# Kernel tuning notes

Hardware: AMD Instinct MI355X
Metric: run time of the kernel (lower is better)

Reference implementation:

```python
import jax, jax.numpy as jnp
import numpy as np

N_AGENTS = 8

def _nearest(x, codebook):
    # x: [N, D], codebook: [K, D] -> indices [N]
    # squared L2 distance via expansion; argmin over codebook axis
    d2 = (jnp.sum(x * x, axis=1, keepdims=True)
          - 2.0 * x @ codebook.T
          + jnp.sum(codebook * codebook, axis=1)[None, :])  # [N, K]
    return jnp.argmin(d2, axis=1)

def setup_inputs() -> dict:
    key = jax.random.key(0)
    ks = jax.random.split(key, 16)
    s = 0.02
    H, D_in, R, K, S = 512, 256, 64, 256, 512
    inp = {
        "inputs": jax.random.normal(ks[0], (131072, D_in), jnp.float32),
        "W0": jax.random.normal(ks[1], (D_in, H), jnp.float32) * s,
        "b0": jnp.zeros((H,), jnp.float32),
        "W1": jax.random.normal(ks[2], (H, H), jnp.float32) * s,
        "b1": jnp.zeros((H,), jnp.float32),
        "W2": jax.random.normal(ks[3], (H, R), jnp.float32) * s,
        "b2": jnp.zeros((R,), jnp.float32),
        "codebook": jax.random.normal(ks[4], (K, R), jnp.float32),
        "W3": jax.random.normal(ks[5], (R, H), jnp.float32) * s,
        "b3": jnp.zeros((H,), jnp.float32),
        "W4": jax.random.normal(ks[6], (N_AGENTS * H, H), jnp.float32) * s,
        "b4": jnp.zeros((H,), jnp.float32),
        "W5": jax.random.normal(ks[7], (H, S), jnp.float32) * s,
        "b5": jnp.zeros((S,), jnp.float32),
    }
    return inp

def reference(inputs, W0, b0, W1, b1, W2, b2, codebook, W3, b3, W4, b4, W5, b5):
    # encode: fc2(relu(fc1(relu(fc0(x)))))
    h = jax.nn.relu(inputs @ W0 + b0)
    h = jax.nn.relu(h @ W1 + b1)
    z_e = h @ W2 + b2  # [N, role_dim]

    # emb(z_e, weight_sg=True): straight-through to z_e, codebook detached
    idx1 = _nearest(z_e, codebook)
    z_q_raw = jnp.take(codebook, idx1, axis=0)
    z_q = z_e + jax.lax.stop_gradient(z_q_raw - z_e)

    # emb(z_e.detach()): grad flows to codebook only (gather -> scatter-add vjp)
    z_e_sg = jax.lax.stop_gradient(z_e)
    idx2 = _nearest(z_e_sg, codebook)
    role_emb = jnp.take(codebook, idx2, axis=0)

    # decode
    rec = jax.nn.relu(z_q @ W3 + b3).reshape(-1, N_AGENTS * W3.shape[1])
    rec = jax.nn.relu(rec @ W4 + b4)
    recon = rec @ W5 + b5  # [N/n_agents, state_dim]
    return recon, z_e, role_emb
```

## Files before the change

kernel.cpp:

```cpp
#include <hip/hip_runtime.h>
#include <hip/hip_bf16.h>
#include <cstddef>

__device__ __forceinline__ unsigned short f2bf(float f) {
    union { float f; unsigned int u; } v; v.f = f;
    unsigned int r = (v.u + 0x7fffu + ((v.u >> 16) & 1u)) >> 16;
    return (unsigned short)r;
}

typedef __bf16    bf16x8 __attribute__((ext_vector_type(8)));
typedef float     f32x4  __attribute__((ext_vector_type(4)));
typedef _Float16  f16x8  __attribute__((ext_vector_type(8)));

#define SPLIT_SCALE 2.44140625e-4f

typedef const __attribute__((address_space(1))) void cglb_t;
typedef __attribute__((address_space(3))) void lds_t;

__device__ __forceinline__ void fsplit(float v, _Float16& hi, _Float16& lo) {
    hi = (_Float16)v;
    lo = (_Float16)((v - (float)hi) * 4096.0f);
}

__device__ __forceinline__ int swz4(int r) { return (r & 3) ^ ((r >> 2) & 3); }

template<int K>
__global__ __launch_bounds__(256, 3)
void gemm_split7(const _Float16* __restrict__ Ahi, const _Float16* __restrict__ Alo,
                 const _Float16* __restrict__ Bhi, const _Float16* __restrict__ Blo,
                 const float* __restrict__ bias,
                 _Float16* __restrict__ Chi, _Float16* __restrict__ Clo,
                 int M, int N)
{
    constexpr int BK = 32;
    constexpr int NS = K / BK;

    __shared__ alignas(16) _Float16 SA[2][2][128 * 32];
    __shared__ alignas(16) _Float16 SB[2][2][64 * 32];

    const int tid  = threadIdx.x;
    const int lane = tid & 63;
    const int w    = tid >> 6;

    int bx = blockIdx.x, by = blockIdx.y;
    {
        const int gx = gridDim.x, nwg = gx * gridDim.y;
        if ((nwg & 7) == 0) {
            int d = bx + by * gx;
            int L = (d & 7) * (nwg >> 3) + (d >> 3);
            bx = L % gx; by = L / gx;
        }
    }
    const int bm = by * 128;
    const int bn = bx * 64;

    f32x4 acc0[2][4], acc1[2][4];
#pragma unroll
    for (int m = 0; m < 2; ++m)
#pragma unroll
        for (int n = 0; n < 4; ++n) {
            acc0[m][n] = (f32x4){0.f, 0.f, 0.f, 0.f};
            acc1[m][n] = (f32x4){0.f, 0.f, 0.f, 0.f};
        }

    auto stage = [&](int buf, int k0) {
#pragma unroll
        for (int pl = 0; pl < 2; ++pl) {
            const _Float16* src = pl ? Alo : Ahi;
#pragma unroll
            for (int j = 0; j < 2; ++j) {
                const int p16 = (w * 2 + j) * 64 + lane;
                const int r   = p16 >> 2;
                const int c   = (p16 & 3) ^ swz4(r);
                const _Float16* g = src + (size_t)(bm + r) * K + k0 + c * 8;
                __builtin_amdgcn_global_load_lds((cglb_t*)g,
                    (lds_t*)&SA[buf][pl][p16 * 8], 16, 0, 0);
            }
            const _Float16* srcB = pl ? Blo : Bhi;
            const int p16b = w * 64 + lane;
            const int rb   = p16b >> 2;
            const int cb   = (p16b & 3) ^ swz4(rb);
            const _Float16* gB = srcB + (size_t)(bn + rb) * K + k0 + cb * 8;
            __builtin_amdgcn_global_load_lds((cglb_t*)gB,
                (lds_t*)&SB[buf][pl][p16b * 8], 16, 0, 0);
        }
    };

    stage(0, 0);
    __syncthreads();

    const int g   = lane >> 4;
    const int r15 = lane & 15;

#pragma unroll
    for (int s = 0; s < NS; ++s) {
        const int p = s & 1;
        if (s + 1 < NS) stage(p ^ 1, (s + 1) * BK);

        f16x8 ah[2], al[2];
#pragma unroll
        for (int m = 0; m < 2; ++m) {
            const int R = w * 32 + m * 16 + r15;
            const int a16 = R * 4 + (g ^ swz4(R));
            ah[m] = *reinterpret_cast<const f16x8*>(&SA[p][0][a16 * 8]);
            al[m] = *reinterpret_cast<const f16x8*>(&SA[p][1][a16 * 8]);
        }
#pragma unroll
        for (int n = 0; n < 4; ++n) {
            const int rB = n * 16 + r15;
            const int b16 = rB * 4 + (g ^ swz4(rB));
            const f16x8 bh = *reinterpret_cast<const f16x8*>(&SB[p][0][b16 * 8]);
            const f16x8 bl = *reinterpret_cast<const f16x8*>(&SB[p][1][b16 * 8]);
#pragma unroll
            for (int m = 0; m < 2; ++m)
                acc0[m][n] = __builtin_amdgcn_mfma_f32_16x16x32_f16(
                    ah[m], bh, acc0[m][n], 0, 0, 0);
#pragma unroll
            for (int m = 0; m < 2; ++m)
                acc1[m][n] = __builtin_amdgcn_mfma_f32_16x16x32_f16(
                    ah[m], bl, acc1[m][n], 0, 0, 0);
#pragma unroll
            for (int m = 0; m < 2; ++m)
                acc1[m][n] = __builtin_amdgcn_mfma_f32_16x16x32_f16(
                    al[m], bh, acc1[m][n], 0, 0, 0);
        }
        __syncthreads();
    }

#pragma unroll
    for (int m = 0; m < 2; ++m)
#pragma unroll
        for (int n = 0; n < 4; ++n) {
            const int col = bn + n * 16 + r15;
            const float bv = bias[col];
#pragma unroll
            for (int q = 0; q < 4; ++q) {
                const int row = bm + w * 32 + m * 16 + (lane >> 4) * 4 + q;
                float v = acc0[m][n][q] + SPLIT_SCALE * acc1[m][n][q] + bv;
                v = fmaxf(v, 0.f);
                _Float16 hi, lo; fsplit(v, hi, lo);
                Chi[(size_t)row * N + col] = hi;
                Clo[(size_t)row * N + col] = lo;
            }
        }
}

template<bool RELU, bool OUT_BF16>
__global__ __launch_bounds__(256, 3)
void gemm_bt7(const unsigned short* __restrict__ A,
              const unsigned short* __restrict__ Bt,
              const float* __restrict__ bias,
              void* __restrict__ Cv, int M, int N, int K)
{
    constexpr int BK = 32;

    __shared__ alignas(16) unsigned short SA[2][128 * 32];
    __shared__ alignas(16) unsigned short SB[2][128 * 32];

    const int tid  = threadIdx.x;
    const int lane = tid & 63;
    const int w    = tid >> 6;
    const int wr   = (w >> 1) * 64;
    const int wc   = (w & 1) * 64;

    int bx = blockIdx.x, by = blockIdx.y;
    {
        const int gx = gridDim.x, nwg = gx * gridDim.y;
        if ((nwg & 7) == 0) {
            int d = bx + by * gx;
            int L = (d & 7) * (nwg >> 3) + (d >> 3);
            bx = L % gx; by = L / gx;
        }
    }
    const int bm = by * 128;
    const int bn = bx * 128;

    f32x4 acc[4][4];
#pragma unroll
    for (int m = 0; m < 4; ++m)
#pragma unroll
        for (int n = 0; n < 4; ++n) acc[m][n] = (f32x4){0.f, 0.f, 0.f, 0.f};

    auto stage = [&](int buf, int k0) {
#pragma unroll
        for (int j = 0; j < 2; ++j) {
            const int p16 = (w * 2 + j) * 64 + lane;
            const int r   = p16 >> 2;
            const int c   = (p16 & 3) ^ swz4(r);
            const unsigned short* gA = A + (size_t)(bm + r) * K + k0 + c * 8;
            __builtin_amdgcn_global_load_lds((cglb_t*)gA,
                (lds_t*)&SA[buf][p16 * 8], 16, 0, 0);
            const unsigned short* gB = Bt + (size_t)(bn + r) * K + k0 + c * 8;
            __builtin_amdgcn_global_load_lds((cglb_t*)gB,
                (lds_t*)&SB[buf][p16 * 8], 16, 0, 0);
        }
    };

    stage(0, 0);
    __syncthreads();

    const int g   = lane >> 4;
    const int r15 = lane & 15;
    const int NS  = K / BK;

    for (int s = 0; s < NS; ++s) {
        const int p = s & 1;
        if (s + 1 < NS) stage(p ^ 1, (s + 1) * BK);

        bf16x8 af[4], bf[4];
#pragma unroll
        for (int m = 0; m < 4; ++m) {
            const int R = wr + m * 16 + r15;
            const int a16 = R * 4 + (g ^ swz4(R));
            af[m] = *reinterpret_cast<const bf16x8*>(&SA[p][a16 * 8]);
        }
#pragma unroll
        for (int n = 0; n < 4; ++n) {
            const int RB = wc + n * 16 + r15;
            const int b16 = RB * 4 + (g ^ swz4(RB));
            bf[n] = *reinterpret_cast<const bf16x8*>(&SB[p][b16 * 8]);
        }
#pragma unroll
        for (int m = 0; m < 4; ++m)
#pragma unroll
            for (int n = 0; n < 4; ++n)
                acc[m][n] = __builtin_amdgcn_mfma_f32_16x16x32_bf16(
                    af[m], bf[n], acc[m][n], 0, 0, 0);
        __syncthreads();
    }

#pragma unroll
    for (int m = 0; m < 4; ++m)
#pragma unroll
        for (int n = 0; n < 4; ++n) {
            const int col = bn + wc + n * 16 + r15;
            const float bv = bias[col];
#pragma unroll
            for (int q = 0; q < 4; ++q) {
                const int row = bm + wr + m * 16 + (lane >> 4) * 4 + q;
                float v = acc[m][n][q] + bv;
                if (RELU) v = fmaxf(v, 0.f);
                if (OUT_BF16)
                    reinterpret_cast<unsigned short*>(Cv)[(size_t)row * N + col] = f2bf(v);
                else
                    reinterpret_cast<float*>(Cv)[(size_t)row * N + col] = v;
            }
        }
}

template<int K, bool AF32>
__global__ __launch_bounds__(256, AF32 ? 3 : 4)
void gemm_split5(const void* __restrict__ Asrc,
                 const _Float16* __restrict__ Bhi, const _Float16* __restrict__ Blo,
                 const float* __restrict__ bias,
                 _Float16* __restrict__ Chi, _Float16* __restrict__ Clo,
                 int M, int N)
{
    constexpr int BK  = 32;
    constexpr int LDP = 40;
    constexpr int NS  = K / BK;

    __shared__ alignas(16) _Float16 Bh[2][64][LDP];
    __shared__ alignas(16) _Float16 Bl[2][64][LDP];

    const int tid  = threadIdx.x;
    const int lane = tid & 63;
    const int w    = tid >> 6;

    int bx = blockIdx.x, by = blockIdx.y;
    {
        const int gx = gridDim.x, nwg = gx * gridDim.y;
        if ((nwg & 7) == 0) {
            int d = bx + by * gx;
            int L = (d & 7) * (nwg >> 3) + (d >> 3);
            bx = L % gx; by = L / gx;
        }
    }
    const int bm = by * 128;
    const int bn = bx * 64;

    f32x4 acc0[2][4], acc1[2][4];
#pragma unroll
    for (int m = 0; m < 2; ++m)
#pragma unroll
        for (int n = 0; n < 4; ++n) {
            acc0[m][n] = (f32x4){0.f, 0.f, 0.f, 0.f};
            acc1[m][n] = (f32x4){0.f, 0.f, 0.f, 0.f};
        }

    const int arow = bm + w * 32 + (lane & 15);
    const int kgrp = (lane >> 4) * 8;
    const int brow = tid >> 2;
    const int bcol = (tid & 3) * 8;

    const _Float16* Ahi_ = (const _Float16*)Asrc;
    const float*    Af_  = (const float*)Asrc;

    f16x8 ah[2], al[2], ahn[2], aln[2];
    float4 rbh, rbl;

    auto loadB = [&](int k0) {
        const size_t gb = (size_t)(bn + brow) * K + k0 + bcol;
        rbh = *reinterpret_cast<const float4*>(Bhi + gb);
        rbl = *reinterpret_cast<const float4*>(Blo + gb);
    };
    auto storeB = [&](int p) {
        *reinterpret_cast<float4*>(&Bh[p][brow][bcol]) = rbh;
        *reinterpret_cast<float4*>(&Bl[p][brow][bcol]) = rbl;
    };
    auto loadA = [&](int k0, f16x8* h, f16x8* l) {
#pragma unroll
        for (int m = 0; m < 2; ++m) {
            const size_t ga = (size_t)(arow + m * 16) * K + k0 + kgrp;
            if constexpr (AF32) {
                float4 v0 = *reinterpret_cast<const float4*>(Af_ + ga);
                float4 v1 = *reinterpret_cast<const float4*>(Af_ + ga + 4);
                float vv[8] = {v0.x, v0.y, v0.z, v0.w, v1.x, v1.y, v1.z, v1.w};
                f16x8 hh, ll;
#pragma unroll
                for (int j = 0; j < 8; ++j) {
                    _Float16 hi, lo; fsplit(vv[j], hi, lo);
                    hh[j] = hi; ll[j] = lo;
                }
                h[m] = hh; l[m] = ll;
            } else {
                h[m] = *reinterpret_cast<const f16x8*>(Ahi_ + ga);
                l[m] = *reinterpret_cast<const f16x8*>(Ahi_ + (size_t)M * K + ga);
            }
        }
    };

    loadB(0);
    loadA(0, ah, al);
    storeB(0);
    __syncthreads();

#pragma unroll
    for (int s = 0; s < NS; ++s) {
        const int p = s & 1;
        if (s + 1 < NS) {
            loadB((s + 1) * BK);
            loadA((s + 1) * BK, ahn, aln);
        }
#pragma unroll
        for (int n = 0; n < 4; ++n) {
            const f16x8 bh = *reinterpret_cast<const f16x8*>(
                &Bh[p][n * 16 + (lane & 15)][kgrp]);
            const f16x8 bl = *reinterpret_cast<const f16x8*>(
                &Bl[p][n * 16 + (lane & 15)][kgrp]);
#pragma unroll
            for (int m = 0; m < 2; ++m)
                acc0[m][n] = __builtin_amdgcn_mfma_f32_16x16x32_f16(
                    ah[m], bh, acc0[m][n], 0, 0, 0);
#pragma unroll
            for (int m = 0; m < 2; ++m)
                acc1[m][n] = __builtin_amdgcn_mfma_f32_16x16x32_f16(
                    ah[m], bl, acc1[m][n], 0, 0, 0);
#pragma unroll
            for (int m = 0; m < 2; ++m)
                acc1[m][n] = __builtin_amdgcn_mfma_f32_16x16x32_f16(
                    al[m], bh, acc1[m][n], 0, 0, 0);
        }
        if (s + 1 < NS) {
            storeB(p ^ 1);
#pragma unroll
            for (int m = 0; m < 2; ++m) { ah[m] = ahn[m]; al[m] = aln[m]; }
        }
        __syncthreads();
    }

#pragma unroll
    for (int m = 0; m < 2; ++m)
#pragma unroll
        for (int n = 0; n < 4; ++n) {
            const int col = bn + n * 16 + (lane & 15);
            const float bv = bias[col];
#pragma unroll
            for (int q = 0; q < 4; ++q) {
                const int row = bm + w * 32 + m * 16 + (lane >> 4) * 4 + q;
                float v = acc0[m][n][q] + SPLIT_SCALE * acc1[m][n][q] + bv;
                v = fmaxf(v, 0.f);
                _Float16 hi, lo; fsplit(v, hi, lo);
                Chi[(size_t)row * N + col] = hi;
                Clo[(size_t)row * N + col] = lo;
            }
        }
}

__global__ __launch_bounds__(256)
void gemm_ze_mfma(const _Float16* __restrict__ Ahi, const _Float16* __restrict__ Alo,
                  const _Float16* __restrict__ Bhi, const _Float16* __restrict__ Blo,
                  const float* __restrict__ bias, float* __restrict__ C, int M)
{
    constexpr int K = 512, N = 64;
    const int tid  = threadIdx.x;
    const int lane = tid & 63;
    const int w    = tid >> 6;
    const int wr   = (w >> 1) * 64;
    const int wc   = (w & 1) * 32;
    const int bm   = blockIdx.x * 128;

    f32x4 acc0[4][2], acc1[4][2];
#pragma unroll
    for (int m = 0; m < 4; ++m)
#pragma unroll
        for (int n = 0; n < 2; ++n) {
            acc0[m][n] = (f32x4){0.f, 0.f, 0.f, 0.f};
            acc1[m][n] = (f32x4){0.f, 0.f, 0.f, 0.f};
        }

    const int arow = bm + wr + (lane & 15);
    const int kgrp = (lane >> 4) * 8;

#pragma unroll
    for (int ks = 0; ks < K / 32; ++ks) {
        const int k0 = ks * 32 + kgrp;
        f16x8 ah[4], al[4];
#pragma unroll
        for (int m = 0; m < 4; ++m) {
            const size_t ga = (size_t)(arow + m * 16) * K + k0;
            ah[m] = *reinterpret_cast<const f16x8*>(Ahi + ga);
            al[m] = *reinterpret_cast<const f16x8*>(Alo + ga);
        }
#pragma unroll
        for (int n = 0; n < 2; ++n) {
            const size_t gb = (size_t)(wc + n * 16 + (lane & 15)) * K + k0;
            const f16x8 bh = *reinterpret_cast<const f16x8*>(Bhi + gb);
            const f16x8 bl = *reinterpret_cast<const f16x8*>(Blo + gb);
#pragma unroll
            for (int m = 0; m < 4; ++m)
                acc0[m][n] = __builtin_amdgcn_mfma_f32_16x16x32_f16(
                    ah[m], bh, acc0[m][n], 0, 0, 0);
#pragma unroll
            for (int m = 0; m < 4; ++m)
                acc1[m][n] = __builtin_amdgcn_mfma_f32_16x16x32_f16(
                    ah[m], bl, acc1[m][n], 0, 0, 0);
#pragma unroll
            for (int m = 0; m < 4; ++m)
                acc1[m][n] = __builtin_amdgcn_mfma_f32_16x16x32_f16(
                    al[m], bh, acc1[m][n], 0, 0, 0);
        }
    }

#pragma unroll
    for (int m = 0; m < 4; ++m)
#pragma unroll
        for (int n = 0; n < 2; ++n) {
            const int col = wc + n * 16 + (lane & 15);
            const float bv = bias[col];
#pragma unroll
            for (int q = 0; q < 4; ++q) {
                const int row = bm + wr + m * 16 + (lane >> 4) * 4 + q;
                C[(size_t)row * N + col] = acc0[m][n][q] + SPLIT_SCALE * acc1[m][n][q] + bv;
            }
        }
}

#define VQ_EPS 1e-3f
__global__ __launch_bounds__(512)
void vq_mfma(const float* __restrict__ Z, const float* __restrict__ CB,
             const _Float16* __restrict__ Chi, const _Float16* __restrict__ Clo,
             float* __restrict__ OUT, unsigned short* __restrict__ ZQB)
{
    __shared__ float  ccf[256];
    __shared__ double ccd[256];
    __shared__ float  xxf[128];
    __shared__ double xxd[128];
    __shared__ float  redv[4][128];
    __shared__ int    redi[4][128];
    __shared__ float  bv1s[128];
    __shared__ int    bis[128];
    __shared__ int    cand[128][16];
    __shared__ int    ncand[128];
    __shared__ int    fullflag[128];
    __shared__ int    flaglist[128];
    __shared__ int    nflag;

    const int tid  = threadIdx.x;
    const int lane = tid & 63;
    const int w    = tid >> 6;
    const int wr   = (w >> 2) * 64;
    const int wc   = (w & 3) * 64;
    const int bm   = blockIdx.x * 128;

    if (tid == 0) nflag = 0;
    if (tid < 256) {
        const float4* c4 = reinterpret_cast<const float4*>(CB + (size_t)tid * 64);
        double cc = 0.0;
#pragma unroll
        for (int v = 0; v < 16; ++v) {
            float4 f = c4[v];
            cc = fma((double)f.x, (double)f.x, cc);
            cc = fma((double)f.y, (double)f.y, cc);
            cc = fma((double)f.z, (double)f.z, cc);
            cc = fma((double)f.w, (double)f.w, cc);
        }
        ccd[tid] = cc; ccf[tid] = (float)cc;
    }
    if (tid < 128) {
        const float4* z4 = reinterpret_cast<const float4*>(Z + (size_t)(bm + tid) * 64);
        double xx = 0.0;
#pragma unroll
        for (int v = 0; v < 16; ++v) {
            float4 f = z4[v];
            xx = fma((double)f.x, (double)f.x, xx);
            xx = fma((double)f.y, (double)f.y, xx);
            xx = fma((double)f.z, (double)f.z, xx);
            xx = fma((double)f.w, (double)f.w, xx);
        }
        xxd[tid] = xx; xxf[tid] = (float)xx;
        ncand[tid] = 0; fullflag[tid] = 0;
    }
    __syncthreads();

    f32x4 acc0[4][4], acc1[4][4];
#pragma unroll
    for (int m = 0; m < 4; ++m)
#pragma unroll
        for (int n = 0; n < 4; ++n) {
            acc0[m][n] = (f32x4){0.f, 0.f, 0.f, 0.f};
            acc1[m][n] = (f32x4){0.f, 0.f, 0.f, 0.f};
        }

    const int arow = bm + wr + (lane & 15);
    const int kgrp = (lane >> 4) * 8;

#pragma unroll
    for (int ks = 0; ks < 2; ++ks) {
        const int k0 = ks * 32 + kgrp;
        f16x8 ah[4], al[4];
#pragma unroll
        for (int m = 0; m < 4; ++m) {
            const float* src = Z + (size_t)(arow + m * 16) * 64 + k0;
            float4 v0 = *reinterpret_cast<const float4*>(src);
            float4 v1 = *reinterpret_cast<const float4*>(src + 4);
            float vv[8] = {v0.x, v0.y, v0.z, v0.w, v1.x, v1.y, v1.z, v1.w};
            f16x8 hh, ll;
#pragma unroll
            for (int j = 0; j < 8; ++j) {
                _Float16 hi, lo; fsplit(vv[j], hi, lo);
                hh[j] = hi; ll[j] = lo;
            }
            ah[m] = hh; al[m] = ll;
        }
#pragma unroll
        for (int n = 0; n < 4; ++n) {
            const size_t gb = (size_t)(wc + n * 16 + (lane & 15)) * 64 + k0;
            const f16x8 bh = *reinterpret_cast<const f16x8*>(Chi + gb);
            const f16x8 bl = *reinterpret_cast<const f16x8*>(Clo + gb);
#pragma unroll
            for (int m = 0; m < 4; ++m)
                acc0[m][n] = __builtin_amdgcn_mfma_f32_16x16x32_f16(
                    ah[m], bh, acc0[m][n], 0, 0, 0);
#pragma unroll
            for (int m = 0; m < 4; ++m)
                acc1[m][n] = __builtin_amdgcn_mfma_f32_16x16x32_f16(
                    ah[m], bl, acc1[m][n], 0, 0, 0);
#pragma unroll
            for (int m = 0; m < 4; ++m)
                acc1[m][n] = __builtin_amdgcn_mfma_f32_16x16x32_f16(
                    al[m], bh, acc1[m][n], 0, 0, 0);
        }
    }

#pragma unroll
    for (int m = 0; m < 4; ++m)
#pragma unroll
        for (int n = 0; n < 4; ++n) {
            const int col = wc + n * 16 + (lane & 15);
            const float cf = ccf[col];
#pragma unroll
            for (int q = 0; q < 4; ++q) {
                const int rl = wr + m * 16 + (lane >> 4) * 4 + q;
                float dot = acc0[m][n][q] + SPLIT_SCALE * acc1[m][n][q];
                acc0[m][n][q] = (xxf[rl] - 2.0f * dot) + cf;
            }
        }

    float bvr[4][4]; int bir[4][4];
#pragma unroll
    for (int m = 0; m < 4; ++m)
#pragma unroll
        for (int q = 0; q < 4; ++q) {
            float bv = 3.4e38f; int bi = 0;
#pragma unroll
            for (int n = 0; n < 4; ++n) {
                const int col = wc + n * 16 + (lane & 15);
                const float v = acc0[m][n][q];
                if (v < bv || (v == bv && col < bi)) { bv = v; bi = col; }
            }
            bvr[m][q] = bv; bir[m][q] = bi;
        }
#pragma unroll
    for (int mask = 1; mask < 16; mask <<= 1) {
#pragma unroll
        for (int m = 0; m < 4; ++m)
#pragma unroll
            for (int q = 0; q < 4; ++q) {
                float ov = __shfl_xor(bvr[m][q], mask);
                int   oi = __shfl_xor(bir[m][q], mask);
                if (ov < bvr[m][q] || (ov == bvr[m][q] && oi < bir[m][q])) {
                    bvr[m][q] = ov; bir[m][q] = oi;
                }
            }
    }
    if ((lane & 15) == 0) {
#pragma unroll
        for (int m = 0; m < 4; ++m)
#pragma unroll
            for (int q = 0; q < 4; ++q) {
                const int rl = wr + m * 16 + (lane >> 4) * 4 + q;
                redv[w & 3][rl] = bvr[m][q];
                redi[w & 3][rl] = bir[m][q];
            }
    }
    __syncthreads();

    if (tid < 128) {
        float bv = 3.4e38f; int bi = 0;
#pragma unroll
        for (int nw = 0; nw < 4; ++nw) {
            float v = redv[nw][tid];
            if (v < bv) { bv = v; bi = redi[nw][tid]; }
        }
        bv1s[tid] = bv; bis[tid] = bi;
    }
    __syncthreads();

#pragma unroll
    for (int m = 0; m < 4; ++m)
#pragma unroll
        for (int q = 0; q < 4; ++q) {
            const int rl = wr + m * 16 + (lane >> 4) * 4 + q;
            const float thr = bv1s[rl] + VQ_EPS;
#pragma unroll
            for (int n = 0; n < 4; ++n) {
                const int col = wc + n * 16 + (lane & 15);
                if (acc0[m][n][q] <= thr) {
                    int s = atomicAdd(&ncand[rl], 1);
                    if (s < 16) cand[rl][s] = col;
                    else        fullflag[rl] = 1;
                }
            }
        }
    __syncthreads();

    if (tid < 128) {
        const int nc_ = ncand[tid] < 16 ? ncand[tid] : 16;
        if (nc_ > 1 && !fullflag[tid]) {
            const float4* z4p = reinterpret_cast<const float4*>(Z + (size_t)(bm + tid) * 64);
            const double xx = xxd[tid];
            double best = 1.0e300; int bi = 256;
            for (int s = 0; s < nc_; ++s) {
                const int e = cand[tid][s];
                const float4* c4p = reinterpret_cast<const float4*>(CB + (size_t)e * 64);
                double dot = 0.0;
#pragma unroll
                for (int v = 0; v < 16; ++v) {
                    float4 zf = z4p[v], cf4 = c4p[v];
                    dot = fma((double)zf.x, (double)cf4.x, dot);
                    dot = fma((double)zf.y, (double)cf4.y, dot);
                    dot = fma((double)zf.z, (double)cf4.z, dot);
                    dot = fma((double)zf.w, (double)cf4.w, dot);
                }
                double d2x = (xx - 2.0 * dot) + ccd[e];
                if (d2x < best || (d2x == best && e < bi)) { best = d2x; bi = e; }
            }
            bis[tid] = bi;
        }
        if (fullflag[tid]) {
            int s = atomicAdd(&nflag, 1);
            flaglist[s] = tid;
        }
    }
    __syncthreads();

    for (int fi = w; fi < nflag; fi += 8) {
        const int rl = flaglist[fi];
        const float* zr = Z + (size_t)(bm + rl) * 64;
        const double xx = xxd[rl];
        double best = 1.0e300; int bi = 256;
#pragma unroll
        for (int j = 0; j < 4; ++j) {
            const int e = lane + j * 64;
            const float* c = CB + (size_t)e * 64;
            double dot = 0.0;
#pragma unroll
            for (int d = 0; d < 64; ++d)
                dot = fma((double)zr[d], (double)c[d], dot);
            double d2x = (xx - 2.0 * dot) + ccd[e];
            if (d2x < best || (d2x == best && e < bi)) { best = d2x; bi = e; }
        }
#pragma unroll
        for (int mask = 1; mask < 64; mask <<= 1) {
            double ov = __shfl_xor(best, mask);
            int    oi = __shfl_xor(bi, mask);
            if (ov < best || (ov == best && oi < bi)) { best = ov; bi = oi; }
        }
        if (lane == 0) bis[rl] = bi;
    }
    __syncthreads();

    {
        const int row  = tid >> 2;
        const int part = tid & 3;
        const int bi   = bis[row];
        const float4* src = reinterpret_cast<const float4*>(CB + (size_t)bi * 64) + part * 4;
        float* dst = OUT + (size_t)(bm + row) * 64 + part * 16;
        unsigned short* dq = ZQB + (size_t)(bm + row) * 64 + part * 16;
#pragma unroll
        for (int v = 0; v < 4; ++v) {
            float4 f = src[v];
            *reinterpret_cast<float4*>(dst + v * 4) = f;
            ushort4 qb = { f2bf(f.x), f2bf(f.y), f2bf(f.z), f2bf(f.w) };
            *reinterpret_cast<ushort4*>(dq + v * 4) = qb;
        }
    }
}

__global__ __launch_bounds__(256)
void transpose_bf16(const float* __restrict__ W, unsigned short* __restrict__ Wt,
                    int K, int N)
{
    int idx = blockIdx.x * 256 + threadIdx.x;
    if (idx >= K * N) return;
    int n = idx / K, k = idx % K;
    Wt[idx] = f2bf(W[(size_t)k * N + n]);
}

__global__ __launch_bounds__(256)
void transpose_split_f16(const float* __restrict__ W,
                         _Float16* __restrict__ Whi, _Float16* __restrict__ Wlo,
                         int K, int N)
{
    int idx = blockIdx.x * 256 + threadIdx.x;
    if (idx >= K * N) return;
    int n = idx / K, k = idx % K;
    _Float16 hi, lo; fsplit(W[(size_t)k * N + n], hi, lo);
    Whi[idx] = hi; Wlo[idx] = lo;
}

__global__ __launch_bounds__(256)
void split_flat_f16(const float* __restrict__ src,
                    _Float16* __restrict__ hi, _Float16* __restrict__ lo, int n)
{
    int i = blockIdx.x * 256 + threadIdx.x;
    if (i >= n) return;
    _Float16 h, l; fsplit(src[i], h, l);
    hi[i] = h; lo[i] = l;
}

extern "C" void kernel_launch(void* const* d_in, const int* in_sizes, int n_in,
                              void* d_out, int out_size, void* d_ws, size_t ws_size,
                              hipStream_t stream)
{
    const float* X  = (const float*)d_in[0];
    const float* W0 = (const float*)d_in[1];
    const float* b0 = (const float*)d_in[2];
    const float* W1 = (const float*)d_in[3];
    const float* b1 = (const float*)d_in[4];
    const float* W2 = (const float*)d_in[5];
    const float* b2 = (const float*)d_in[6];
    const float* CB = (const float*)d_in[7];
    const float* W3 = (const float*)d_in[8];
    const float* b3 = (const float*)d_in[9];
    const float* W4 = (const float*)d_in[10];
    const float* b4 = (const float*)d_in[11];
    const float* W5 = (const float*)d_in[12];
    const float* b5 = (const float*)d_in[13];

    const int D_in = 256, H = 512, R = 64, S = 512, NA = 8;
    const int Mtot = in_sizes[0] / D_in;

    float* recon = (float*)d_out;
    float* ze    = recon + (size_t)(Mtot / NA) * S;
    float* remb  = ze + (size_t)Mtot * R;

    char* p = (char*)d_ws;
    _Float16* W0hi = (_Float16*)p;  p += (size_t)H * D_in * 2;
    _Float16* W0lo = (_Float16*)p;  p += (size_t)H * D_in * 2;
    _Float16* W1hi = (_Float16*)p;  p += (size_t)H * H * 2;
    _Float16* W1lo = (_Float16*)p;  p += (size_t)H * H * 2;
    _Float16* W2thi = (_Float16*)p; p += (size_t)R * H * 2;
    _Float16* W2tlo = (_Float16*)p; p += (size_t)R * H * 2;
    _Float16* CBhi = (_Float16*)p;  p += (size_t)256 * R * 2;
    _Float16* CBlo = (_Float16*)p;  p += (size_t)256 * R * 2;
    unsigned short* W3t = (unsigned short*)p;  p += (size_t)H * R * 2;
    unsigned short* W4t = (unsigned short*)p;  p += (size_t)H * (NA * H) * 2;
    unsigned short* W5t = (unsigned short*)p;  p += (size_t)S * H * 2;
    size_t fixed = (size_t)(p - (char*)d_ws);
    fixed = (fixed + 255) & ~(size_t)255;

    int nc = 1;
    while (nc < 128) {
        size_t rpcT = (size_t)Mtot / nc;
        if (fixed + rpcT * 4224 + 1024 <= ws_size) break;
        nc *= 2;
    }
    const int rpc = Mtot / nc;
    char* q = (char*)d_ws + fixed;
    _Float16* h0hi = (_Float16*)q;                 q += (size_t)rpc * H * 2;
    _Float16* h0lo = (_Float16*)q;                 q += (size_t)rpc * H * 2;
    _Float16* h1hi = (_Float16*)q;                 q += (size_t)rpc * H * 2;
    _Float16* h1lo = (_Float16*)q;                 q += (size_t)rpc * H * 2;
    unsigned short* zqb = (unsigned short*)q;      q += (size_t)rpc * R * 2;
    unsigned short* rec1b = (unsigned short*)h0hi;
    unsigned short* rec2b = (unsigned short*)h1hi;

    transpose_split_f16<<<(H * D_in + 255) / 256, 256, 0, stream>>>(W0, W0hi, W0lo, D_in, H);
    transpose_split_f16<<<(H * H + 255) / 256, 256, 0, stream>>>(W1, W1hi, W1lo, H, H);
    transpose_split_f16<<<(H * R + 255) / 256, 256, 0, stream>>>(W2, W2thi, W2tlo, H, R);
    split_flat_f16<<<(256 * R + 255) / 256, 256, 0, stream>>>(CB, CBhi, CBlo, 256 * R);
    transpose_bf16<<<(H * R + 255) / 256, 256, 0, stream>>>(W3, W3t, R, H);
    transpose_bf16<<<(H * NA * H + 255) / 256, 256, 0, stream>>>(W4, W4t, NA * H, H);
    transpose_bf16<<<(S * H + 255) / 256, 256, 0, stream>>>(W5, W5t, H, S);

    for (int r0 = 0; r0 < Mtot; r0 += rpc) {
        const int M6 = rpc / NA;
        gemm_split5<256, true><<<dim3(H / 64, rpc / 128), 256, 0, stream>>>(
            X + (size_t)r0 * D_in, W0hi, W0lo, b0, h0hi, h0lo, rpc, H);
        gemm_split7<512><<<dim3(H / 64, rpc / 128), 256, 0, stream>>>(
            h0hi, h0lo, W1hi, W1lo, b1, h1hi, h1lo, rpc, H);
        gemm_ze_mfma<<<rpc / 128, 256, 0, stream>>>(
            h1hi, h1lo, W2thi, W2tlo, b2, ze + (size_t)r0 * R, rpc);
        vq_mfma<<<rpc / 128, 512, 0, stream>>>(
            ze + (size_t)r0 * R, CB, CBhi, CBlo,
            remb + (size_t)r0 * R, zqb);
        gemm_bt7<true, true><<<dim3(H / 128, rpc / 128), 256, 0, stream>>>(
            zqb, W3t, b3, rec1b, rpc, H, R);
        gemm_bt7<true, true><<<dim3(H / 128, M6 / 128), 256, 0, stream>>>(
            rec1b, W4t, b4, rec2b, M6, H, NA * H);
        gemm_bt7<false, false><<<dim3(S / 128, M6 / 128), 256, 0, stream>>>(
            rec2b, W5t, b5, recon + (size_t)(r0 / NA) * S, M6, S, H);
    }
}
```

Baseline: 945.8 us.

## Stage fp32 A tiles through swizzled LDS for first layer; split decode into larger chunks

After: 855.0 us. -9.6%, faster.

```diff
diff --git a/kernel.cpp b/kernel.cpp
--- a/kernel.cpp
+++ b/kernel.cpp
@@ -145,6 +145,151 @@
         }
 }
 
+__global__ __launch_bounds__(256, 3)
+void gemm_split7f(const float* __restrict__ Af,
+                  const _Float16* __restrict__ Bhi, const _Float16* __restrict__ Blo,
+                  const float* __restrict__ bias,
+                  _Float16* __restrict__ Chi, _Float16* __restrict__ Clo,
+                  int M, int N)
+{
+    constexpr int K  = 256;
+    constexpr int BK = 32;
+    constexpr int NS = K / BK;
+
+    __shared__ alignas(16) _Float16 SA[2][2][128 * 32];
+    __shared__ alignas(16) _Float16 SB[2][2][64 * 32];
+
+    const int tid  = threadIdx.x;
+    const int lane = tid & 63;
+    const int w    = tid >> 6;
+
+    int bx = blockIdx.x, by = blockIdx.y;
+    {
+        const int gx = gridDim.x, nwg = gx * gridDim.y;
+        if ((nwg & 7) == 0) {
+            int d = bx + by * gx;
+            int L = (d & 7) * (nwg >> 3) + (d >> 3);
+            bx = L % gx; by = L / gx;
+        }
+    }
+    const int bm = by * 128;
+    const int bn = bx * 64;
+
+    f32x4 acc0[2][4], acc1[2][4];
+#pragma unroll
+    for (int m = 0; m < 2; ++m)
+#pragma unroll
+        for (int n = 0; n < 4; ++n) {
+            acc0[m][n] = (f32x4){0.f, 0.f, 0.f, 0.f};
+            acc1[m][n] = (f32x4){0.f, 0.f, 0.f, 0.f};
+        }
+
+    float4 ra[2][2];
+    auto loadA = [&](int k0) {
+#pragma unroll
+        for (int j = 0; j < 2; ++j) {
+            const int p16 = tid * 2 + j;
+            const int r   = p16 >> 2;
+            const int c   = (p16 & 3) ^ swz4(r);
+            const float* g = Af + (size_t)(bm + r) * K + k0 + c * 8;
+            ra[j][0] = *reinterpret_cast<const float4*>(g);
+            ra[j][1] = *reinterpret_cast<const float4*>(g + 4);
+        }
+    };
+    auto writeA = [&](int buf) {
+#pragma unroll
+        for (int j = 0; j < 2; ++j) {
+            const int p16 = tid * 2 + j;
+            float vv[8] = {ra[j][0].x, ra[j][0].y, ra[j][0].z, ra[j][0].w,
+                           ra[j][1].x, ra[j][1].y, ra[j][1].z, ra[j][1].w};
+            f16x8 hh, ll;
+#pragma unroll
+            for (int e = 0; e < 8; ++e) {
+                _Float16 hi, lo; fsplit(vv[e], hi, lo);
+                hh[e] = hi; ll[e] = lo;
+            }
+            *reinterpret_cast<f16x8*>(&SA[buf][0][p16 * 8]) = hh;
+            *reinterpret_cast<f16x8*>(&SA[buf][1][p16 * 8]) = ll;
+        }
+    };
+    auto stageB = [&](int buf, int k0) {
+#pragma unroll
+        for (int pl = 0; pl < 2; ++pl) {
+            const _Float16* srcB = pl ? Blo : Bhi;
+            const int p16b = w * 64 + lane;
+            const int rb   = p16b >> 2;
+            const int cb   = (p16b & 3) ^ swz4(rb);
+            const _Float16* gB = srcB + (size_t)(bn + rb) * K + k0 + cb * 8;
+            __builtin_amdgcn_global_load_lds((cglb_t*)gB,
+                (lds_t*)&SB[buf][pl][p16b * 8], 16, 0, 0);
+        }
+    };
+
+    loadA(0);
+    stageB(0, 0);
+    writeA(0);
+    __syncthreads();
+
+    const int g   = lane >> 4;
+    const int r15 = lane & 15;
+
+#pragma unroll
+    for (int s = 0; s < NS; ++s) {
+        const int p = s & 1;
+        if (s + 1 < NS) {
+            stageB(p ^ 1, (s + 1) * BK);
+            loadA((s + 1) * BK);
+        }
+
+        f16x8 ah[2], al[2];
+#pragma unroll
+        for (int m = 0; m < 2; ++m) {
+            const int R = w * 32 + m * 16 + r15;
+            const int a16 = R * 4 + (g ^ swz4(R));
+            ah[m] = *reinterpret_cast<const f16x8*>(&SA[p][0][a16 * 8]);
+            al[m] = *reinterpret_cast<const f16x8*>(&SA[p][1][a16 * 8]);
+        }
+#pragma unroll
+        for (int n = 0; n < 4; ++n) {
+            const int rB = n * 16 + r15;
+            const int b16 = rB * 4 + (g ^ swz4(rB));
+            const f16x8 bh = *reinterpret_cast<const f16x8*>(&SB[p][0][b16 * 8]);
+            const f16x8 bl = *reinterpret_cast<const f16x8*>(&SB[p][1][b16 * 8]);
+#pragma unroll
+            for (int m = 0; m < 2; ++m)
+                acc0[m][n] = __builtin_amdgcn_mfma_f32_16x16x32_f16(
+                    ah[m], bh, acc0[m][n], 0, 0, 0);
+#pragma unroll
+            for (int m = 0; m < 2; ++m)
+                acc1[m][n] = __builtin_amdgcn_mfma_f32_16x16x32_f16(
+                    ah[m], bl, acc1[m][n], 0, 0, 0);
+#pragma unroll
+            for (int m = 0; m < 2; ++m)
+                acc1[m][n] = __builtin_amdgcn_mfma_f32_16x16x32_f16(
+                    al[m], bh, acc1[m][n], 0, 0, 0);
+        }
+        if (s + 1 < NS) writeA(p ^ 1);
+        __syncthreads();
+    }
+
+#pragma unroll
+    for (int m = 0; m < 2; ++m)
+#pragma unroll
+        for (int n = 0; n < 4; ++n) {
+            const int col = bn + n * 16 + r15;
+            const float bv = bias[col];
+#pragma unroll
+            for (int q = 0; q < 4; ++q) {
+                const int row = bm + w * 32 + m * 16 + (lane >> 4) * 4 + q;
+                float v = acc0[m][n][q] + SPLIT_SCALE * acc1[m][n][q] + bv;
+                v = fmaxf(v, 0.f);
+                _Float16 hi, lo; fsplit(v, hi, lo);
+                Chi[(size_t)row * N + col] = hi;
+                Clo[(size_t)row * N + col] = lo;
+            }
+        }
+}
+
 template<bool RELU, bool OUT_BF16>
 __global__ __launch_bounds__(256, 3)
 void gemm_bt7(const unsigned short* __restrict__ A,
@@ -244,145 +389,6 @@
                     reinterpret_cast<unsigned short*>(Cv)[(size_t)row * N + col] = f2bf(v);
                 else
                     reinterpret_cast<float*>(Cv)[(size_t)row * N + col] = v;
-            }
-        }
-}
-
-template<int K, bool AF32>
-__global__ __launch_bounds__(256, AF32 ? 3 : 4)
-void gemm_split5(const void* __restrict__ Asrc,
-                 const _Float16* __restrict__ Bhi, const _Float16* __restrict__ Blo,
-                 const float* __restrict__ bias,
-                 _Float16* __restrict__ Chi, _Float16* __restrict__ Clo,
-                 int M, int N)
-{
-    constexpr int BK  = 32;
-    constexpr int LDP = 40;
-    constexpr int NS  = K / BK;
-
-    __shared__ alignas(16) _Float16 Bh[2][64][LDP];
-    __shared__ alignas(16) _Float16 Bl[2][64][LDP];
-
-    const int tid  = threadIdx.x;
-    const int lane = tid & 63;
-    const int w    = tid >> 6;
-
-    int bx = blockIdx.x, by = blockIdx.y;
-    {
-        const int gx = gridDim.x, nwg = gx * gridDim.y;
-        if ((nwg & 7) == 0) {
-            int d = bx + by * gx;
-            int L = (d & 7) * (nwg >> 3) + (d >> 3);
-            bx = L % gx; by = L / gx;
-        }
-    }
-    const int bm = by * 128;
-    const int bn = bx * 64;
-
-    f32x4 acc0[2][4], acc1[2][4];
-#pragma unroll
-    for (int m = 0; m < 2; ++m)
-#pragma unroll
-        for (int n = 0; n < 4; ++n) {
-            acc0[m][n] = (f32x4){0.f, 0.f, 0.f, 0.f};
-            acc1[m][n] = (f32x4){0.f, 0.f, 0.f, 0.f};
-        }
-
-    const int arow = bm + w * 32 + (lane & 15);
-    const int kgrp = (lane >> 4) * 8;
-    const int brow = tid >> 2;
-    const int bcol = (tid & 3) * 8;
-
-    const _Float16* Ahi_ = (const _Float16*)Asrc;
-    const float*    Af_  = (const float*)Asrc;
-
-    f16x8 ah[2], al[2], ahn[2], aln[2];
-    float4 rbh, rbl;
-
-    auto loadB = [&](int k0) {
-        const size_t gb = (size_t)(bn + brow) * K + k0 + bcol;
-        rbh = *reinterpret_cast<const float4*>(Bhi + gb);
-        rbl = *reinterpret_cast<const float4*>(Blo + gb);
-    };
-    auto storeB = [&](int p) {
-        *reinterpret_cast<float4*>(&Bh[p][brow][bcol]) = rbh;
-        *reinterpret_cast<float4*>(&Bl[p][brow][bcol]) = rbl;
-    };
-    auto loadA = [&](int k0, f16x8* h, f16x8* l) {
-#pragma unroll
-        for (int m = 0; m < 2; ++m) {
-            const size_t ga = (size_t)(arow + m * 16) * K + k0 + kgrp;
-            if constexpr (AF32) {
-                float4 v0 = *reinterpret_cast<const float4*>(Af_ + ga);
-                float4 v1 = *reinterpret_cast<const float4*>(Af_ + ga + 4);
-                float vv[8] = {v0.x, v0.y, v0.z, v0.w, v1.x, v1.y, v1.z, v1.w};
-                f16x8 hh, ll;
-#pragma unroll
-                for (int j = 0; j < 8; ++j) {
-                    _Float16 hi, lo; fsplit(vv[j], hi, lo);
-                    hh[j] = hi; ll[j] = lo;
-                }
-                h[m] = hh; l[m] = ll;
-            } else {
-                h[m] = *reinterpret_cast<const f16x8*>(Ahi_ + ga);
-                l[m] = *reinterpret_cast<const f16x8*>(Ahi_ + (size_t)M * K + ga);
-            }
-        }
-    };
-
-    loadB(0);
-    loadA(0, ah, al);
-    storeB(0);
-    __syncthreads();
-
-#pragma unroll
-    for (int s = 0; s < NS; ++s) {
-        const int p = s & 1;
-        if (s + 1 < NS) {
-            loadB((s + 1) * BK);
-            loadA((s + 1) * BK, ahn, aln);
-        }
-#pragma unroll
-        for (int n = 0; n < 4; ++n) {
-            const f16x8 bh = *reinterpret_cast<const f16x8*>(
-                &Bh[p][n * 16 + (lane & 15)][kgrp]);
-            const f16x8 bl = *reinterpret_cast<const f16x8*>(
-                &Bl[p][n * 16 + (lane & 15)][kgrp]);
-#pragma unroll
-            for (int m = 0; m < 2; ++m)
-                acc0[m][n] = __builtin_amdgcn_mfma_f32_16x16x32_f16(
-                    ah[m], bh, acc0[m][n], 0, 0, 0);
-#pragma unroll
-            for (int m = 0; m < 2; ++m)
-                acc1[m][n] = __builtin_amdgcn_mfma_f32_16x16x32_f16(
-                    ah[m], bl, acc1[m][n], 0, 0, 0);
-#pragma unroll
-            for (int m = 0; m < 2; ++m)
-                acc1[m][n] = __builtin_amdgcn_mfma_f32_16x16x32_f16(
-                    al[m], bh, acc1[m][n], 0, 0, 0);
-        }
-        if (s + 1 < NS) {
-            storeB(p ^ 1);
-#pragma unroll
-            for (int m = 0; m < 2; ++m) { ah[m] = ahn[m]; al[m] = aln[m]; }
-        }
-        __syncthreads();
-    }
-
-#pragma unroll
-    for (int m = 0; m < 2; ++m)
-#pragma unroll
-        for (int n = 0; n < 4; ++n) {
-            const int col = bn + n * 16 + (lane & 15);
-            const float bv = bias[col];
-#pragma unroll
-            for (int q = 0; q < 4; ++q) {
-                const int row = bm + w * 32 + m * 16 + (lane >> 4) * 4 + q;
-                float v = acc0[m][n][q] + SPLIT_SCALE * acc1[m][n][q] + bv;
-                v = fmaxf(v, 0.f);
-                _Float16 hi, lo; fsplit(v, hi, lo);
-                Chi[(size_t)row * N + col] = hi;
-                Clo[(size_t)row * N + col] = lo;
             }
         }
 }
@@ -788,24 +794,29 @@
     unsigned short* W3t = (unsigned short*)p;  p += (size_t)H * R * 2;
     unsigned short* W4t = (unsigned short*)p;  p += (size_t)H * (NA * H) * 2;
     unsigned short* W5t = (unsigned short*)p;  p += (size_t)S * H * 2;
+    unsigned short* zqb = (unsigned short*)p;  p += (size_t)Mtot * R * 2;
     size_t fixed = (size_t)(p - (char*)d_ws);
     fixed = (fixed + 255) & ~(size_t)255;
 
     int nc = 1;
     while (nc < 128) {
         size_t rpcT = (size_t)Mtot / nc;
-        if (fixed + rpcT * 4224 + 1024 <= ws_size) break;
+        if (fixed + rpcT * 4096 + 1024 <= ws_size) break;
         nc *= 2;
     }
     const int rpc = Mtot / nc;
-    char* q = (char*)d_ws + fixed;
-    _Float16* h0hi = (_Float16*)q;                 q += (size_t)rpc * H * 2;
-    _Float16* h0lo = (_Float16*)q;                 q += (size_t)rpc * H * 2;
-    _Float16* h1hi = (_Float16*)q;                 q += (size_t)rpc * H * 2;
-    _Float16* h1lo = (_Float16*)q;                 q += (size_t)rpc * H * 2;
-    unsigned short* zqb = (unsigned short*)q;      q += (size_t)rpc * R * 2;
-    unsigned short* rec1b = (unsigned short*)h0hi;
-    unsigned short* rec2b = (unsigned short*)h1hi;
+    char* regionA = (char*)d_ws + fixed;
+    char* regionB = regionA + (size_t)rpc * 2048;
+
+    _Float16* h1hi = (_Float16*)regionA;
+    _Float16* h1lo = h1hi + (size_t)rpc * H;
+    _Float16* h0hi = (_Float16*)regionB;
+    _Float16* h0lo = h0hi + (size_t)rpc * H;
+
+    int dc = (nc >= 2) ? nc / 2 : 1;
+    const int Mdec = Mtot / dc;
+    unsigned short* rec1b = (unsigned short*)regionB;
+    unsigned short* rec2b = (unsigned short*)regionA;
 
     transpose_split_f16<<<(H * D_in + 255) / 256, 256, 0, stream>>>(W0, W0hi, W0lo, D_in, H);
     transpose_split_f16<<<(H * H + 255) / 256, 256, 0, stream>>>(W1, W1hi, W1lo, H, H);
@@ -816,8 +827,7 @@
     transpose_bf16<<<(S * H + 255) / 256, 256, 0, stream>>>(W5, W5t, H, S);
 
     for (int r0 = 0; r0 < Mtot; r0 += rpc) {
-        const int M6 = rpc / NA;
-        gemm_split5<256, true><<<dim3(H / 64, rpc / 128), 256, 0, stream>>>(
+        gemm_split7f<<<dim3(H / 64, rpc / 128), 256, 0, stream>>>(
             X + (size_t)r0 * D_in, W0hi, W0lo, b0, h0hi, h0lo, rpc, H);
         gemm_split7<512><<<dim3(H / 64, rpc / 128), 256, 0, stream>>>(
             h0hi, h0lo, W1hi, W1lo, b1, h1hi, h1lo, rpc, H);
@@ -825,9 +835,13 @@
             h1hi, h1lo, W2thi, W2tlo, b2, ze + (size_t)r0 * R, rpc);
         vq_mfma<<<rpc / 128, 512, 0, stream>>>(
             ze + (size_t)r0 * R, CB, CBhi, CBlo,
-            remb + (size_t)r0 * R, zqb);
-        gemm_bt7<true, true><<<dim3(H / 128, rpc / 128), 256, 0, stream>>>(
-            zqb, W3t, b3, rec1b, rpc, H, R);
+            remb + (size_t)r0 * R, zqb + (size_t)r0 * R);
+    }
+
+    for (int r0 = 0; r0 < Mtot; r0 += Mdec) {
+        const int M6 = Mdec / NA;
+        gemm_bt7<true, true><<<dim3(H / 128, Mdec / 128), 256, 0, stream>>>(
+            zqb + (size_t)r0 * R, W3t, b3, rec1b, Mdec, H, R);
         gemm_bt7<true, true><<<dim3(H / 128, M6 / 128), 256, 0, stream>>>(
             rec1b, W4t, b4, rec2b, M6, H, NA * H);
         gemm_bt7<false, false><<<dim3(S / 128, M6 / 128), 256, 0, stream>>>(
```
